# Performance work log

Measured on AMD Instinct MI355X. Metric: run time of the kernel, lower is better.

The kernel has to match this reference:

```python
import jax, jax.numpy as jnp
import numpy as np

B, L, HS, WS = 4, 5, 32, 32
C = 256            # dim == heads * dim_head
M, D = 8, 32       # heads, dim_head
T, R = 2, 4        # num_types, num_relations
I = M * D          # inner_dim
EPS = 1e-5


def setup_inputs() -> dict:
    key = jax.random.key(0)
    ks = jax.random.split(key, 12)
    w = 0.02
    x = jax.random.normal(ks[0], (B, L, HS, WS, C), dtype=jnp.float32)
    mask = jnp.ones((B, HS, WS, L, L), dtype=jnp.int32)
    prior_encoding = jax.random.randint(ks[1], (B, L, HS, WS, 3), 0, T).astype(jnp.float32)
    return {
        "x": x,
        "mask": mask,
        "prior_encoding": prior_encoding,
        "ln_w": jnp.ones((C,), jnp.float32),
        "ln_b": jnp.zeros((C,), jnp.float32),
        "Wq": jax.random.normal(ks[2], (T, C, I), jnp.float32) * w,
        "bq": jnp.zeros((T, I), jnp.float32),
        "Wk": jax.random.normal(ks[3], (T, C, I), jnp.float32) * w,
        "bk": jnp.zeros((T, I), jnp.float32),
        "Wv": jax.random.normal(ks[4], (T, C, I), jnp.float32) * w,
        "bv": jnp.zeros((T, I), jnp.float32),
        "Wa": jax.random.normal(ks[5], (T, I, C), jnp.float32) * w,
        "ba": jnp.zeros((T, C), jnp.float32),
        "rel_att": jax.random.normal(ks[6], (R, M, D, D), jnp.float32) * w,
        "rel_msg": jax.random.normal(ks[7], (R, M, D, D), jnp.float32) * w,
    }


def _hgt_forward(x, mask, prior_encoding, ln_w, ln_b, Wq, bq, Wk, bk, Wv, bv, Wa, ba, rel_att, rel_msg):
    # pre-LayerNorm over channel dim
    mu = jnp.mean(x, axis=-1, keepdims=True)
    var = jnp.mean(jnp.square(x - mu), axis=-1, keepdims=True)
    xn = (x - mu) * jax.lax.rsqrt(var + EPS) * ln_w + ln_b

    # [B,L,H,W,C] -> [B,H,W,L,C]
    xp = jnp.transpose(xn, (0, 2, 3, 1, 4))
    types = prior_encoding[:, :, 0, 0, 2].astype(jnp.int32)  # [B,L]

    # per-type q/k/v projections via gather of type-indexed weights
    q = jnp.einsum('bhwlc,blci->bhwli', xp, Wq[types]) + bq[types][:, None, None]
    k = jnp.einsum('bhwlc,blci->bhwli', xp, Wk[types]) + bk[types][:, None, None]
    v = jnp.einsum('bhwlc,blci->bhwli', xp, Wv[types]) + bv[types][:, None, None]

    def to_heads(t):  # [B,H,W,L,I] -> [B,M,H,W,L,D]
        return jnp.transpose(t.reshape(B, HS, WS, L, M, D), (0, 4, 1, 2, 3, 5))
    q, k, v = to_heads(q), to_heads(k), to_heads(v)

    # relation-indexed edge weights: e_type = t_i * T + t_j
    e = types[:, :, None] * T + types[:, None, :]              # [B,L,L]
    w_att = jnp.transpose(rel_att[e], (0, 3, 1, 2, 4, 5))      # [B,M,L,L,D,D]
    w_msg = jnp.transpose(rel_msg[e], (0, 3, 1, 2, 4, 5))

    scale = D ** -0.5
    q_w = jnp.einsum('bmhwip,bmijpq->bmhwijq', q, w_att)
    att = jnp.einsum('bmhwijq,bmhwjq->bmhwij', q_w, k) * scale
    att = jnp.where(mask[:, None] == 0, -1e9, att)
    att = jax.nn.softmax(att, axis=-1)

    v_msg = jnp.einsum('bmijpc,bmhwjp->bmhwijc', w_msg, v)
    out = jnp.einsum('bmhwij,bmhwijc->bmhwic', att, v_msg)

    # [B,M,H,W,L,D] -> [B,H,W,L,C]
    out = jnp.transpose(out, (0, 2, 3, 4, 1, 5)).reshape(B, HS, WS, L, I)
    out = jnp.einsum('bhwli,blic->bhwlc', out, Wa[types]) + ba[types][:, None, None]
    # dropout is identity at inference
    return jnp.transpose(out, (0, 3, 1, 2, 4))                 # [B,L,H,W,C]


def reference(x, mask, prior_encoding, ln_w, ln_b, Wq, bq, Wk, bk, Wv, bv, Wa, ba, rel_att, rel_msg):
    return _hgt_forward(x, mask, prior_encoding, ln_w, ln_b, Wq, bq, Wk, bk, Wv, bv, Wa, ba, rel_att, rel_msg)
```

## Files before the change

kernel.cpp:

```cpp
#include <hip/hip_runtime.h>
#include <hip/hip_bf16.h>
#include <math.h>

#define BB 4
#define LL 5
#define HSZ 32
#define WSZ 32
#define PP (HSZ*WSZ)
#define CC 256
#define MM 8
#define DD 32
#define II 256
#define TT 2
#define NTOK (BB*PP*LL*II)
#define TILE_ELEMS 8192
#define SCALE 0.17677669529663687f

typedef short bf16x8 __attribute__((ext_vector_type(8)));
typedef float f32x4 __attribute__((ext_vector_type(4)));

static __device__ __forceinline__ ushort f2bf(float f) {
    unsigned u = __float_as_uint(f);
    unsigned r = (u + 0x7fffu + ((u >> 16) & 1u)) >> 16;
    return (ushort)r;
}
static __device__ __forceinline__ float bf2f(ushort u) {
    return __uint_as_float(((unsigned)u) << 16);
}

__global__ __launch_bounds__(256) void k_fold(
    const float* __restrict__ Wq, const float* __restrict__ Wv,
    const float* __restrict__ Wk, const float* __restrict__ Wa,
    const float* __restrict__ bq, const float* __restrict__ bv,
    const float* __restrict__ rel_att, const float* __restrict__ rel_msg,
    const float* __restrict__ x,
    const float* __restrict__ lnw, const float* __restrict__ lnb,
    ushort* __restrict__ packW, float* __restrict__ bEff,
    ushort* __restrict__ xnPack)
{
    __shared__ float As[1024];
    __shared__ ushort Apack[8192];
    const int blk = blockIdx.x;
    const int tid = threadIdx.x;

    if (blk < 64) {
        const int p  = blk >> 5;
        const int t  = (blk >> 4) & 1;
        const int ts = (blk >> 3) & 1;
        const int m  = blk & 7;
        const float* A = (p == 0)
            ? rel_att + (size_t)((t * 2 + ts) * 8 + m) * 1024
            : rel_msg + (size_t)((ts * 2 + t) * 8 + m) * 1024;
        for (int i = tid; i < 1024; i += 256) As[i] = A[i];
        __syncthreads();

        const float* W = ((p == 0) ? Wq : Wv) + (size_t)t * 65536;
        const int k = tid;
        float wrow[32];
        #pragma unroll
        for (int u = 0; u < 8; ++u)
            *(float4*)&wrow[u * 4] = *(const float4*)&W[k * 256 + m * 32 + u * 4];

        const int slot = (p == 0 ? 0 : 4) + t * 2 + ts;
        ushort* base = packW + (size_t)slot * 65536;
        const int kt = k >> 5, j = k & 7, lq = ((k >> 3) & 3) * 16;
        #pragma unroll
        for (int q = 0; q < 32; ++q) {
            float acc = 0.f;
            #pragma unroll
            for (int pp = 0; pp < 32; ++pp) acc += wrow[pp] * As[pp * 32 + q];
            const int nt = m * 2 + (q >> 4);
            const int lane = lq + (q & 15);
            base[(size_t)((nt * 8 + kt) * 64 + lane) * 8 + j] = f2bf(acc);
        }
        if (tid < 32) {
            const int q = tid;
            const float* bi = ((p == 0) ? bq : bv) + t * 256 + m * 32;
            float acc = 0.f;
            #pragma unroll
            for (int pp = 0; pp < 32; ++pp) acc += bi[pp] * As[pp * 32 + q];
            bEff[(p ? 1024 : 0) + (t * 2 + ts) * 256 + m * 32 + q] = acc;
        }
    } else if (blk < 192) {
        const int idx = blk - 64;
        const int which = idx >> 6;
        const int gi = (idx & 63) * 256 + tid;
        const int t = gi >> 13;
        const int sub = gi & 8191;
        const float* src = ((which == 0) ? Wk : Wa) + (size_t)t * 65536;
        const int slot = (which == 0 ? 8 : 10) + t;
        const int nt = sub >> 9, kt = (sub >> 6) & 7, lane = sub & 63;
        const int k0 = kt * 32 + (lane >> 4) * 8;
        const int n  = nt * 16 + (lane & 15);
        ushort h[8];
        #pragma unroll
        for (int j = 0; j < 8; ++j) h[j] = f2bf(src[(size_t)(k0 + j) * 256 + n]);
        uint4 o;
        o.x = (unsigned)h[0] | ((unsigned)h[1] << 16);
        o.y = (unsigned)h[2] | ((unsigned)h[3] << 16);
        o.z = (unsigned)h[4] | ((unsigned)h[5] << 16);
        o.w = (unsigned)h[6] | ((unsigned)h[7] << 16);
        *(uint4*)(packW + (size_t)slot * 65536 + (size_t)sub * 8) = o;
    } else {
        const int lblk = blk - 192;
        const int bl  = lblk >> 5;
        const int pt  = lblk & 31;
        const int p0  = pt * 32;

        const int r  = tid >> 3;
        const int jj = tid & 7;
        const float* xrow = x + ((size_t)bl * PP + p0 + r) * CC;
        float4 xv[8];
        float s1 = 0.f, s2 = 0.f;
        #pragma unroll
        for (int u = 0; u < 8; ++u) {
            xv[u] = *(const float4*)(xrow + jj * 32 + u * 4);
            s1 += xv[u].x + xv[u].y + xv[u].z + xv[u].w;
            s2 += xv[u].x * xv[u].x + xv[u].y * xv[u].y + xv[u].z * xv[u].z + xv[u].w * xv[u].w;
        }
        s1 += __shfl_xor(s1, 1); s1 += __shfl_xor(s1, 2); s1 += __shfl_xor(s1, 4);
        s2 += __shfl_xor(s2, 1); s2 += __shfl_xor(s2, 2); s2 += __shfl_xor(s2, 4);
        const float mu   = s1 * (1.0f / 256.0f);
        const float var  = s2 * (1.0f / 256.0f) - mu * mu;
        const float rstd = rsqrtf(var + 1e-5f);

        const int mt_r = r >> 4, rm = r & 15;
        #pragma unroll
        for (int u = 0; u < 8; ++u) {
            const int c0 = jj * 32 + u * 4;
            const float4 g  = *(const float4*)(lnw + c0);
            const float4 bt = *(const float4*)(lnb + c0);
            const ushort h0 = f2bf((xv[u].x - mu) * rstd * g.x + bt.x);
            const ushort h1 = f2bf((xv[u].y - mu) * rstd * g.y + bt.y);
            const ushort h2 = f2bf((xv[u].z - mu) * rstd * g.z + bt.z);
            const ushort h3 = f2bf((xv[u].w - mu) * rstd * g.w + bt.w);
            uint2 w2;
            w2.x = (unsigned)h0 | ((unsigned)h1 << 16);
            w2.y = (unsigned)h2 | ((unsigned)h3 << 16);
            const int kt   = c0 >> 5;
            const int lsub = rm + (((c0 >> 3) & 3) << 4);
            const int j0   = c0 & 7;
            *(uint2*)&Apack[(((mt_r * 8 + kt) * 64 + lsub) << 3) + j0] = w2;
        }
        __syncthreads();

        const size_t tbase = (size_t)lblk * TILE_ELEMS;
        #pragma unroll
        for (int u = 0; u < 4; ++u) {
            const int ch = (tid + u * 256) * 8;
            *(uint4*)&xnPack[tbase + ch] = *(const uint4*)&Apack[ch];
        }
    }
}

__global__ __launch_bounds__(256) void k_proj(
    const ushort* __restrict__ xnPack, const float* __restrict__ prior,
    const ushort* __restrict__ packW, const float* __restrict__ bEff,
    const float* __restrict__ bk,
    ushort* __restrict__ qw0, ushort* __restrict__ qw1, ushort* __restrict__ kkO,
    ushort* __restrict__ vm0, ushort* __restrict__ vm1)
{
    __shared__ ushort As[8192];

    const int tid  = threadIdx.x;
    const int blk  = blockIdx.x;
    const int mat  = blk / 640;
    const int rem  = blk - mat * 640;
    const int bl   = rem >> 5;
    const int sub  = rem & 31;
    const int pg   = sub >> 1;
    const int half = sub & 1;
    const int t    = (int)prior[(size_t)bl * (PP * 3) + 2];

    int slot; const float* bias;
    if (mat < 2)       { slot = t * 2 + mat;           bias = bEff + slot * 256; }
    else if (mat == 2) { slot = 8 + t;                 bias = bk + t * 256; }
    else               { slot = 4 + t * 2 + (mat - 3); bias = bEff + 1024 + (t * 2 + (mat - 3)) * 256; }
    ushort* dst = (mat == 0) ? qw0 : (mat == 1) ? qw1 : (mat == 2) ? kkO : (mat == 3) ? vm0 : vm1;

    const int wv = tid >> 6, lane = tid & 63;

    const ushort* Bp = packW + (size_t)slot * 65536;
    bf16x8 bfr[8][2];
    #pragma unroll
    for (int kt = 0; kt < 8; ++kt)
        #pragma unroll
        for (int nn = 0; nn < 2; ++nn) {
            const int ntg = half * 8 + wv * 2 + nn;
            bfr[kt][nn] = *(const bf16x8*)&Bp[(size_t)((ntg * 8 + kt) * 64 + lane) * 8];
        }

    const int cl = lane & 15, rq = lane >> 4;
    const int colA = half * 128 + wv * 32 + cl;
    const int colB = colA + 16;
    const float biasA = bias[colA], biasB = bias[colB];

    #pragma unroll 1
    for (int tl = 0; tl < 2; ++tl) {
        const int pt = pg * 2 + tl;
        const size_t tbase = (size_t)(bl * 32 + pt) * TILE_ELEMS;
        __syncthreads();
        #pragma unroll
        for (int u = 0; u < 4; ++u) {
            const int ch = (tid + u * 256) * 8;
            *(uint4*)&As[ch] = *(const uint4*)&xnPack[tbase + ch];
        }
        __syncthreads();

        f32x4 acc[2][2];
        #pragma unroll
        for (int mt = 0; mt < 2; ++mt)
            #pragma unroll
            for (int nn = 0; nn < 2; ++nn)
                acc[mt][nn] = (f32x4){0.f, 0.f, 0.f, 0.f};

        #pragma unroll
        for (int kt = 0; kt < 8; ++kt) {
            const bf16x8 a0 = *(const bf16x8*)&As[((0 * 8 + kt) * 64 + lane) << 3];
            const bf16x8 a1 = *(const bf16x8*)&As[((1 * 8 + kt) * 64 + lane) << 3];
            acc[0][0] = __builtin_amdgcn_mfma_f32_16x16x32_bf16(a0, bfr[kt][0], acc[0][0], 0, 0, 0);
            acc[0][1] = __builtin_amdgcn_mfma_f32_16x16x32_bf16(a0, bfr[kt][1], acc[0][1], 0, 0, 0);
            acc[1][0] = __builtin_amdgcn_mfma_f32_16x16x32_bf16(a1, bfr[kt][0], acc[1][0], 0, 0, 0);
            acc[1][1] = __builtin_amdgcn_mfma_f32_16x16x32_bf16(a1, bfr[kt][1], acc[1][1], 0, 0, 0);
        }

        const int p0 = pt * 32;
        #pragma unroll
        for (int mt = 0; mt < 2; ++mt) {
            const int row0 = p0 + mt * 16 + rq * 4;
            #pragma unroll
            for (int r2 = 0; r2 < 4; ++r2) {
                const size_t rb = ((size_t)bl * PP + row0 + r2) * II;
                dst[rb + colA] = f2bf(acc[mt][0][r2] + biasA);
                dst[rb + colB] = f2bf(acc[mt][1][r2] + biasB);
            }
        }
    }
}

__global__ __launch_bounds__(256) void k_attn_lite(
    const ushort* __restrict__ qw0, const ushort* __restrict__ qw1,
    const ushort* __restrict__ kkI,
    const ushort* __restrict__ vm0, const ushort* __restrict__ vm1,
    const int* __restrict__ mask, const float* __restrict__ prior,
    ushort* __restrict__ aoPack)
{
    const int tid  = threadIdx.x;
    const int site = blockIdx.x * 4 + (tid >> 6);
    const int lane = tid & 63;
    const int b    = site >> 10;
    const int pix  = site & 1023;
    const int c0   = lane * 4;

    int ty[5];
    #pragma unroll
    for (int l = 0; l < 5; ++l)
        ty[l] = (int)prior[(size_t)(b * 5 + l) * (PP * 3) + 2];

    float qf[2][5][4], kf[5][4], vf[2][5][4];
    #pragma unroll
    for (int l = 0; l < 5; ++l) {
        const size_t base = (((size_t)(b * 5 + l) << 10) + pix) * II + c0;
        const ushort4 q0 = *(const ushort4*)(qw0 + base);
        const ushort4 q1 = *(const ushort4*)(qw1 + base);
        const ushort4 kv = *(const ushort4*)(kkI + base);
        const ushort4 v0 = *(const ushort4*)(vm0 + base);
        const ushort4 v1 = *(const ushort4*)(vm1 + base);
        qf[0][l][0] = bf2f(q0.x); qf[0][l][1] = bf2f(q0.y); qf[0][l][2] = bf2f(q0.z); qf[0][l][3] = bf2f(q0.w);
        qf[1][l][0] = bf2f(q1.x); qf[1][l][1] = bf2f(q1.y); qf[1][l][2] = bf2f(q1.z); qf[1][l][3] = bf2f(q1.w);
        kf[l][0]    = bf2f(kv.x); kf[l][1]    = bf2f(kv.y); kf[l][2]    = bf2f(kv.z); kf[l][3]    = bf2f(kv.w);
        vf[0][l][0] = bf2f(v0.x); vf[0][l][1] = bf2f(v0.y); vf[0][l][2] = bf2f(v0.z); vf[0][l][3] = bf2f(v0.w);
        vf[1][l][0] = bf2f(v1.x); vf[1][l][1] = bf2f(v1.y); vf[1][l][2] = bf2f(v1.z); vf[1][l][3] = bf2f(v1.w);
    }

    const int rr   = pix & 31;
    const int tile0 = b * 5 * 32 + (pix >> 5);
    const int mt   = rr >> 4;
    const int ktc  = c0 >> 5;
    const int lp   = (rr & 15) + 16 * ((c0 >> 3) & 3);
    const int j0   = c0 & 7;
    const int fofs = ((mt * 8 + ktc) * 64 + lp) * 8 + j0;

    #pragma unroll
    for (int i = 0; i < 5; ++i) {
        float lg[5];
        #pragma unroll
        for (int j = 0; j < 5; ++j) {
            const float s0 = qf[0][i][0] * kf[j][0] + qf[0][i][1] * kf[j][1]
                           + qf[0][i][2] * kf[j][2] + qf[0][i][3] * kf[j][3];
            const float s1 = qf[1][i][0] * kf[j][0] + qf[1][i][1] * kf[j][1]
                           + qf[1][i][2] * kf[j][2] + qf[1][i][3] * kf[j][3];
            float s = ty[j] ? s1 : s0;
            s += __shfl_xor(s, 1); s += __shfl_xor(s, 2); s += __shfl_xor(s, 4);
            const int mv = mask[((size_t)site * 5 + i) * 5 + j];
            lg[j] = mv ? s * SCALE : -1e9f;
        }
        float mx = lg[0];
        #pragma unroll
        for (int j = 1; j < 5; ++j) mx = fmaxf(mx, lg[j]);
        float ex[5], sum = 0.f;
        #pragma unroll
        for (int j = 0; j < 5; ++j) { ex[j] = __expf(lg[j] - mx); sum += ex[j]; }
        const float rs = 1.0f / sum;
        float o0 = 0.f, o1 = 0.f, o2 = 0.f, o3 = 0.f;
        #pragma unroll
        for (int j = 0; j < 5; ++j) {
            const float w = ex[j] * rs;
            o0 += w * (ty[i] ? vf[1][j][0] : vf[0][j][0]);
            o1 += w * (ty[i] ? vf[1][j][1] : vf[0][j][1]);
            o2 += w * (ty[i] ? vf[1][j][2] : vf[0][j][2]);
            o3 += w * (ty[i] ? vf[1][j][3] : vf[0][j][3]);
        }
        uint2 w2;
        w2.x = (unsigned)f2bf(o0) | ((unsigned)f2bf(o1) << 16);
        w2.y = (unsigned)f2bf(o2) | ((unsigned)f2bf(o3) << 16);
        *(uint2*)&aoPack[(size_t)(tile0 + i * 32) * TILE_ELEMS + fofs] = w2;
    }
}

__global__ __launch_bounds__(256) void k_out(
    const ushort* __restrict__ aoPack, const float* __restrict__ prior,
    const ushort* __restrict__ packW, const float* __restrict__ ba,
    float* __restrict__ out)
{
    __shared__ ushort As[8192];
    __shared__ float obufF[32 * 132];

    const int tid  = threadIdx.x;
    const int blk  = blockIdx.x;
    const int bl   = blk >> 6;
    const int sub  = blk & 63;
    const int pt   = sub >> 1;
    const int half = sub & 1;
    const int bbi  = bl / LL;
    const int l    = bl - bbi * LL;
    const int t    = (int)prior[(size_t)bl * (PP * 3) + 2];

    const int wv = tid >> 6, lane = tid & 63;
    const ushort* Bp = packW + (size_t)(10 + t) * 65536;
    bf16x8 bfr[8][2];
    #pragma unroll
    for (int kt = 0; kt < 8; ++kt)
        #pragma unroll
        for (int nn = 0; nn < 2; ++nn) {
            const int ntg = half * 8 + wv * 2 + nn;
            bfr[kt][nn] = *(const bf16x8*)&Bp[(size_t)((ntg * 8 + kt) * 64 + lane) * 8];
        }

    const size_t tbase = (size_t)(bl * 32 + pt) * TILE_ELEMS;
    #pragma unroll
    for (int u = 0; u < 4; ++u) {
        const int ch = (tid + u * 256) * 8;
        *(uint4*)&As[ch] = *(const uint4*)&aoPack[tbase + ch];
    }
    __syncthreads();

    const int cl = lane & 15, rq = lane >> 4;
    const int colL_A = wv * 32 + cl;
    const int colL_B = colL_A + 16;
    const float biasA = ba[t * CC + half * 128 + colL_A];
    const float biasB = ba[t * CC + half * 128 + colL_B];

    f32x4 acc[2][2];
    #pragma unroll
    for (int mt = 0; mt < 2; ++mt)
        #pragma unroll
        for (int nn = 0; nn < 2; ++nn)
            acc[mt][nn] = (f32x4){0.f, 0.f, 0.f, 0.f};

    #pragma unroll
    for (int kt = 0; kt < 8; ++kt) {
        const bf16x8 a0 = *(const bf16x8*)&As[((0 * 8 + kt) * 64 + lane) << 3];
        const bf16x8 a1 = *(const bf16x8*)&As[((1 * 8 + kt) * 64 + lane) << 3];
        acc[0][0] = __builtin_amdgcn_mfma_f32_16x16x32_bf16(a0, bfr[kt][0], acc[0][0], 0, 0, 0);
        acc[0][1] = __builtin_amdgcn_mfma_f32_16x16x32_bf16(a0, bfr[kt][1], acc[0][1], 0, 0, 0);
        acc[1][0] = __builtin_amdgcn_mfma_f32_16x16x32_bf16(a1, bfr[kt][0], acc[1][0], 0, 0, 0);
        acc[1][1] = __builtin_amdgcn_mfma_f32_16x16x32_bf16(a1, bfr[kt][1], acc[1][1], 0, 0, 0);
    }

    #pragma unroll
    for (int mt = 0; mt < 2; ++mt) {
        const int rowb = mt * 16 + rq * 4;
        #pragma unroll
        for (int r2 = 0; r2 < 4; ++r2) {
            obufF[(rowb + r2) * 132 + colL_A] = acc[mt][0][r2] + biasA;
            obufF[(rowb + r2) * 132 + colL_B] = acc[mt][1][r2] + biasB;
        }
    }
    __syncthreads();

    const int p0 = pt * 32;
    #pragma unroll
    for (int k2 = 0; k2 < 4; ++k2) {
        const int id  = tid + k2 * 256;
        const int row = id >> 5;
        const int ch  = (id & 31) * 4;
        const float4 v4 = *(const float4*)&obufF[row * 132 + ch];
        *(float4*)(out + ((size_t)(bbi * LL + l) * PP + p0 + row) * CC + half * 128 + ch) = v4;
    }
}

extern "C" void kernel_launch(void* const* d_in, const int* in_sizes, int n_in,
                              void* d_out, int out_size, void* d_ws, size_t ws_size,
                              hipStream_t stream) {
    const float* x       = (const float*)d_in[0];
    const int*   mask    = (const int*)d_in[1];
    const float* prior   = (const float*)d_in[2];
    const float* lnw     = (const float*)d_in[3];
    const float* lnb     = (const float*)d_in[4];
    const float* Wq      = (const float*)d_in[5];
    const float* bq      = (const float*)d_in[6];
    const float* Wk      = (const float*)d_in[7];
    const float* bk      = (const float*)d_in[8];
    const float* Wv      = (const float*)d_in[9];
    const float* bv      = (const float*)d_in[10];
    const float* Wa      = (const float*)d_in[11];
    const float* ba      = (const float*)d_in[12];
    const float* rel_att = (const float*)d_in[13];
    const float* rel_msg = (const float*)d_in[14];
    float* out = (float*)d_out;

    ushort* qw0    = (ushort*)d_ws;
    ushort* qw1    = qw0 + NTOK;
    ushort* kko    = qw1 + NTOK;
    ushort* vm0    = kko + NTOK;
    ushort* vm1    = vm0 + NTOK;
    ushort* aoPack = vm1 + NTOK;
    ushort* xnPack = aoPack + NTOK;
    ushort* packW  = xnPack + NTOK;
    float*  bEff   = (float*)(packW + 12 * 65536);

    hipLaunchKernelGGL(k_fold, dim3(832), dim3(256), 0, stream,
                       Wq, Wv, Wk, Wa, bq, bv, rel_att, rel_msg,
                       x, lnw, lnb, packW, bEff, xnPack);
    hipLaunchKernelGGL(k_proj, dim3(3200), dim3(256), 0, stream,
                       xnPack, prior, packW, bEff, bk, qw0, qw1, kko, vm0, vm1);
    hipLaunchKernelGGL(k_attn_lite, dim3(1024), dim3(256), 0, stream,
                       qw0, qw1, kko, vm0, vm1, mask, prior, aoPack);
    hipLaunchKernelGGL(k_out, dim3(1280), dim3(256), 0, stream,
                       aoPack, prior, packW, ba, out);
}
```

Before: 150.1 us.

## Fuse attention and output projection into one kernel via block-local staging

Merges the attention kernel and the output-projection kernel into a single launch. Each 512-thread block computes attention for 16 pixels across all 5 positions, writes the bf16 result to a block-private global scratch tile, then runs the MFMA output projection on that tile after a block barrier. This removes one kernel launch and keeps the intermediate likely cache-resident. In exchange the grid drops to 256 blocks, B weights are re-read from global each loop instead of kept in registers, and the output is stored with scattered scalar writes rather than staged float4 stores.

```diff
diff --git a/kernel.cpp b/kernel.cpp
--- a/kernel.cpp
+++ b/kernel.cpp
@@ -238,165 +238,124 @@
     }
 }
 
-__global__ __launch_bounds__(256) void k_attn_lite(
+__global__ __launch_bounds__(512) void k_attn_out(
     const ushort* __restrict__ qw0, const ushort* __restrict__ qw1,
     const ushort* __restrict__ kkI,
     const ushort* __restrict__ vm0, const ushort* __restrict__ vm1,
     const int* __restrict__ mask, const float* __restrict__ prior,
-    ushort* __restrict__ aoPack)
+    const ushort* __restrict__ packW, const float* __restrict__ ba,
+    ushort* __restrict__ aoG, float* __restrict__ out)
 {
+    __shared__ int tys[8];
+
     const int tid  = threadIdx.x;
-    const int site = blockIdx.x * 4 + (tid >> 6);
+    const int wv   = tid >> 6;
     const int lane = tid & 63;
-    const int b    = site >> 10;
-    const int pix  = site & 1023;
-    const int c0   = lane * 4;
-
-    int ty[5];
-    #pragma unroll
-    for (int l = 0; l < 5; ++l)
-        ty[l] = (int)prior[(size_t)(b * 5 + l) * (PP * 3) + 2];
-
-    float qf[2][5][4], kf[5][4], vf[2][5][4];
-    #pragma unroll
-    for (int l = 0; l < 5; ++l) {
-        const size_t base = (((size_t)(b * 5 + l) << 10) + pix) * II + c0;
-        const ushort4 q0 = *(const ushort4*)(qw0 + base);
-        const ushort4 q1 = *(const ushort4*)(qw1 + base);
-        const ushort4 kv = *(const ushort4*)(kkI + base);
-        const ushort4 v0 = *(const ushort4*)(vm0 + base);
-        const ushort4 v1 = *(const ushort4*)(vm1 + base);
-        qf[0][l][0] = bf2f(q0.x); qf[0][l][1] = bf2f(q0.y); qf[0][l][2] = bf2f(q0.z); qf[0][l][3] = bf2f(q0.w);
-        qf[1][l][0] = bf2f(q1.x); qf[1][l][1] = bf2f(q1.y); qf[1][l][2] = bf2f(q1.z); qf[1][l][3] = bf2f(q1.w);
-        kf[l][0]    = bf2f(kv.x); kf[l][1]    = bf2f(kv.y); kf[l][2]    = bf2f(kv.z); kf[l][3]    = bf2f(kv.w);
-        vf[0][l][0] = bf2f(v0.x); vf[0][l][1] = bf2f(v0.y); vf[0][l][2] = bf2f(v0.z); vf[0][l][3] = bf2f(v0.w);
-        vf[1][l][0] = bf2f(v1.x); vf[1][l][1] = bf2f(v1.y); vf[1][l][2] = bf2f(v1.z); vf[1][l][3] = bf2f(v1.w);
+    const int blk  = blockIdx.x;
+    const int b    = blk >> 6;
+    const int p0   = (blk & 63) * 16;
+
+    if (tid < 5) tys[tid] = (int)prior[(size_t)(b * 5 + tid) * (PP * 3) + 2];
+    __syncthreads();
+
+    const int c0 = lane * 4;
+    const int ktc  = lane >> 3;
+    const int lpc  = 16 * ((lane >> 1) & 3);
+    const int j0   = 4 * (lane & 1);
+
+    #pragma unroll 1
+    for (int ss = 0; ss < 2; ++ss) {
+        const int pixl = wv * 2 + ss;
+        const int pix  = p0 + pixl;
+        const size_t siteg = (size_t)b * PP + pix;
+
+        float qf[2][5][4], kf[5][4], vf[2][5][4];
+        #pragma unroll
+        for (int l = 0; l < 5; ++l) {
+            const size_t base = (((size_t)(b * 5 + l) << 10) + pix) * II + c0;
+            const ushort4 q0 = *(const ushort4*)(qw0 + base);
+            const ushort4 q1 = *(const ushort4*)(qw1 + base);
+            const ushort4 kv = *(const ushort4*)(kkI + base);
+            const ushort4 v0 = *(const ushort4*)(vm0 + base);
+            const ushort4 v1 = *(const ushort4*)(vm1 + base);
+            qf[0][l][0] = bf2f(q0.x); qf[0][l][1] = bf2f(q0.y); qf[0][l][2] = bf2f(q0.z); qf[0][l][3] = bf2f(q0.w);
+            qf[1][l][0] = bf2f(q1.x); qf[1][l][1] = bf2f(q1.y); qf[1][l][2] = bf2f(q1.z); qf[1][l][3] = bf2f(q1.w);
+            kf[l][0]    = bf2f(kv.x); kf[l][1]    = bf2f(kv.y); kf[l][2]    = bf2f(kv.z); kf[l][3]    = bf2f(kv.w);
+            vf[0][l][0] = bf2f(v0.x); vf[0][l][1] = bf2f(v0.y); vf[0][l][2] = bf2f(v0.z); vf[0][l][3] = bf2f(v0.w);
+            vf[1][l][0] = bf2f(v1.x); vf[1][l][1] = bf2f(v1.y); vf[1][l][2] = bf2f(v1.z); vf[1][l][3] = bf2f(v1.w);
+        }
+
+        #pragma unroll
+        for (int i = 0; i < 5; ++i) {
+            float lg[5];
+            #pragma unroll
+            for (int j = 0; j < 5; ++j) {
+                const float s0 = qf[0][i][0] * kf[j][0] + qf[0][i][1] * kf[j][1]
+                               + qf[0][i][2] * kf[j][2] + qf[0][i][3] * kf[j][3];
+                const float s1 = qf[1][i][0] * kf[j][0] + qf[1][i][1] * kf[j][1]
+                               + qf[1][i][2] * kf[j][2] + qf[1][i][3] * kf[j][3];
+                float s = tys[j] ? s1 : s0;
+                s += __shfl_xor(s, 1); s += __shfl_xor(s, 2); s += __shfl_xor(s, 4);
+                const int mv = mask[(siteg * 5 + i) * 5 + j];
+                lg[j] = mv ? s * SCALE : -1e9f;
+            }
+            float mx = lg[0];
+            #pragma unroll
+            for (int j = 1; j < 5; ++j) mx = fmaxf(mx, lg[j]);
+            float ex[5], sum = 0.f;
+            #pragma unroll
+            for (int j = 0; j < 5; ++j) { ex[j] = __expf(lg[j] - mx); sum += ex[j]; }
+            const float rs = 1.0f / sum;
+            float o0 = 0.f, o1 = 0.f, o2 = 0.f, o3 = 0.f;
+            #pragma unroll
+            for (int j = 0; j < 5; ++j) {
+                const float w = ex[j] * rs;
+                o0 += w * (tys[i] ? vf[1][j][0] : vf[0][j][0]);
+                o1 += w * (tys[i] ? vf[1][j][1] : vf[0][j][1]);
+                o2 += w * (tys[i] ? vf[1][j][2] : vf[0][j][2]);
+                o3 += w * (tys[i] ? vf[1][j][3] : vf[0][j][3]);
+            }
+            uint2 w2;
+            w2.x = (unsigned)f2bf(o0) | ((unsigned)f2bf(o1) << 16);
+            w2.y = (unsigned)f2bf(o2) | ((unsigned)f2bf(o3) << 16);
+            const size_t elem = (size_t)blk * 20480 + (size_t)i * 4096
+                              + (size_t)((ktc * 64) + (pixl + lpc)) * 8 + j0;
+            *(uint2*)&aoG[elem] = w2;
+        }
     }
 
-    const int rr   = pix & 31;
-    const int tile0 = b * 5 * 32 + (pix >> 5);
-    const int mt   = rr >> 4;
-    const int ktc  = c0 >> 5;
-    const int lp   = (rr & 15) + 16 * ((c0 >> 3) & 3);
-    const int j0   = c0 & 7;
-    const int fofs = ((mt * 8 + ktc) * 64 + lp) * 8 + j0;
-
-    #pragma unroll
-    for (int i = 0; i < 5; ++i) {
-        float lg[5];
-        #pragma unroll
-        for (int j = 0; j < 5; ++j) {
-            const float s0 = qf[0][i][0] * kf[j][0] + qf[0][i][1] * kf[j][1]
-                           + qf[0][i][2] * kf[j][2] + qf[0][i][3] * kf[j][3];
-            const float s1 = qf[1][i][0] * kf[j][0] + qf[1][i][1] * kf[j][1]
-                           + qf[1][i][2] * kf[j][2] + qf[1][i][3] * kf[j][3];
-            float s = ty[j] ? s1 : s0;
-            s += __shfl_xor(s, 1); s += __shfl_xor(s, 2); s += __shfl_xor(s, 4);
-            const int mv = mask[((size_t)site * 5 + i) * 5 + j];
-            lg[j] = mv ? s * SCALE : -1e9f;
-        }
-        float mx = lg[0];
-        #pragma unroll
-        for (int j = 1; j < 5; ++j) mx = fmaxf(mx, lg[j]);
-        float ex[5], sum = 0.f;
-        #pragma unroll
-        for (int j = 0; j < 5; ++j) { ex[j] = __expf(lg[j] - mx); sum += ex[j]; }
-        const float rs = 1.0f / sum;
-        float o0 = 0.f, o1 = 0.f, o2 = 0.f, o3 = 0.f;
-        #pragma unroll
-        for (int j = 0; j < 5; ++j) {
-            const float w = ex[j] * rs;
-            o0 += w * (ty[i] ? vf[1][j][0] : vf[0][j][0]);
-            o1 += w * (ty[i] ? vf[1][j][1] : vf[0][j][1]);
-            o2 += w * (ty[i] ? vf[1][j][2] : vf[0][j][2]);
-            o3 += w * (ty[i] ? vf[1][j][3] : vf[0][j][3]);
-        }
-        uint2 w2;
-        w2.x = (unsigned)f2bf(o0) | ((unsigned)f2bf(o1) << 16);
-        w2.y = (unsigned)f2bf(o2) | ((unsigned)f2bf(o3) << 16);
-        *(uint2*)&aoPack[(size_t)(tile0 + i * 32) * TILE_ELEMS + fofs] = w2;
-    }
-}
-
-__global__ __launch_bounds__(256) void k_out(
-    const ushort* __restrict__ aoPack, const float* __restrict__ prior,
-    const ushort* __restrict__ packW, const float* __restrict__ ba,
-    float* __restrict__ out)
-{
-    __shared__ ushort As[8192];
-    __shared__ float obufF[32 * 132];
-
-    const int tid  = threadIdx.x;
-    const int blk  = blockIdx.x;
-    const int bl   = blk >> 6;
-    const int sub  = blk & 63;
-    const int pt   = sub >> 1;
-    const int half = sub & 1;
-    const int bbi  = bl / LL;
-    const int l    = bl - bbi * LL;
-    const int t    = (int)prior[(size_t)bl * (PP * 3) + 2];
-
-    const int wv = tid >> 6, lane = tid & 63;
-    const ushort* Bp = packW + (size_t)(10 + t) * 65536;
-    bf16x8 bfr[8][2];
-    #pragma unroll
-    for (int kt = 0; kt < 8; ++kt)
-        #pragma unroll
-        for (int nn = 0; nn < 2; ++nn) {
-            const int ntg = half * 8 + wv * 2 + nn;
-            bfr[kt][nn] = *(const bf16x8*)&Bp[(size_t)((ntg * 8 + kt) * 64 + lane) * 8];
-        }
-
-    const size_t tbase = (size_t)(bl * 32 + pt) * TILE_ELEMS;
-    #pragma unroll
-    for (int u = 0; u < 4; ++u) {
-        const int ch = (tid + u * 256) * 8;
-        *(uint4*)&As[ch] = *(const uint4*)&aoPack[tbase + ch];
-    }
+    __threadfence_block();
     __syncthreads();
 
     const int cl = lane & 15, rq = lane >> 4;
-    const int colL_A = wv * 32 + cl;
-    const int colL_B = colL_A + 16;
-    const float biasA = ba[t * CC + half * 128 + colL_A];
-    const float biasB = ba[t * CC + half * 128 + colL_B];
-
-    f32x4 acc[2][2];
-    #pragma unroll
-    for (int mt = 0; mt < 2; ++mt)
-        #pragma unroll
-        for (int nn = 0; nn < 2; ++nn)
-            acc[mt][nn] = (f32x4){0.f, 0.f, 0.f, 0.f};
-
-    #pragma unroll
-    for (int kt = 0; kt < 8; ++kt) {
-        const bf16x8 a0 = *(const bf16x8*)&As[((0 * 8 + kt) * 64 + lane) << 3];
-        const bf16x8 a1 = *(const bf16x8*)&As[((1 * 8 + kt) * 64 + lane) << 3];
-        acc[0][0] = __builtin_amdgcn_mfma_f32_16x16x32_bf16(a0, bfr[kt][0], acc[0][0], 0, 0, 0);
-        acc[0][1] = __builtin_amdgcn_mfma_f32_16x16x32_bf16(a0, bfr[kt][1], acc[0][1], 0, 0, 0);
-        acc[1][0] = __builtin_amdgcn_mfma_f32_16x16x32_bf16(a1, bfr[kt][0], acc[1][0], 0, 0, 0);
-        acc[1][1] = __builtin_amdgcn_mfma_f32_16x16x32_bf16(a1, bfr[kt][1], acc[1][1], 0, 0, 0);
-    }
-
-    #pragma unroll
-    for (int mt = 0; mt < 2; ++mt) {
-        const int rowb = mt * 16 + rq * 4;
+    #pragma unroll 1
+    for (int g = wv; g < 40; g += 8) {
+        const int mt  = g >> 3;
+        const int ntp = g & 7;
+        const int t   = tys[mt];
+        const ushort* Bp = packW + (size_t)(10 + t) * 65536;
+        const ushort* Ap = aoG + (size_t)blk * 20480 + (size_t)mt * 4096;
+        const int nt0 = ntp * 2, nt1 = nt0 + 1;
+
+        f32x4 acc0 = (f32x4){0.f, 0.f, 0.f, 0.f};
+        f32x4 acc1 = (f32x4){0.f, 0.f, 0.f, 0.f};
+        #pragma unroll
+        for (int kt = 0; kt < 8; ++kt) {
+            const bf16x8 a  = *(const bf16x8*)&Ap[(size_t)(kt * 64 + lane) * 8];
+            const bf16x8 b0 = *(const bf16x8*)&Bp[(size_t)((nt0 * 8 + kt) * 64 + lane) * 8];
+            const bf16x8 b1 = *(const bf16x8*)&Bp[(size_t)((nt1 * 8 + kt) * 64 + lane) * 8];
+            acc0 = __builtin_amdgcn_mfma_f32_16x16x32_bf16(a, b0, acc0, 0, 0, 0);
+            acc1 = __builtin_amdgcn_mfma_f32_16x16x32_bf16(a, b1, acc1, 0, 0, 0);
+        }
+
+        const float bias0 = ba[t * CC + nt0 * 16 + cl];
+        const float bias1 = ba[t * CC + nt1 * 16 + cl];
+        float* ob = out + ((size_t)(b * 5 + mt) * PP + p0 + rq * 4) * CC;
         #pragma unroll
         for (int r2 = 0; r2 < 4; ++r2) {
-            obufF[(rowb + r2) * 132 + colL_A] = acc[mt][0][r2] + biasA;
-            obufF[(rowb + r2) * 132 + colL_B] = acc[mt][1][r2] + biasB;
-        }
-    }
-    __syncthreads();
-
-    const int p0 = pt * 32;
-    #pragma unroll
-    for (int k2 = 0; k2 < 4; ++k2) {
-        const int id  = tid + k2 * 256;
-        const int row = id >> 5;
-        const int ch  = (id & 31) * 4;
-        const float4 v4 = *(const float4*)&obufF[row * 132 + ch];
-        *(float4*)(out + ((size_t)(bbi * LL + l) * PP + p0 + row) * CC + half * 128 + ch) = v4;
+            ob[(size_t)r2 * CC + nt0 * 16 + cl] = acc0[r2] + bias0;
+            ob[(size_t)r2 * CC + nt1 * 16 + cl] = acc1[r2] + bias1;
+        }
     }
 }
 
@@ -425,8 +384,8 @@
     ushort* kko    = qw1 + NTOK;
     ushort* vm0    = kko + NTOK;
     ushort* vm1    = vm0 + NTOK;
-    ushort* aoPack = vm1 + NTOK;
-    ushort* xnPack = aoPack + NTOK;
+    ushort* aoG    = vm1 + NTOK;
+    ushort* xnPack = aoG + NTOK;
     ushort* packW  = xnPack + NTOK;
     float*  bEff   = (float*)(packW + 12 * 65536);
 
@@ -435,8 +394,6 @@
                        x, lnw, lnb, packW, bEff, xnPack);
     hipLaunchKernelGGL(k_proj, dim3(3200), dim3(256), 0, stream,
                        xnPack, prior, packW, bEff, bk, qw0, qw1, kko, vm0, vm1);
-    hipLaunchKernelGGL(k_attn_lite, dim3(1024), dim3(256), 0, stream,
-                       qw0, qw1, kko, vm0, vm1, mask, prior, aoPack);
-    hipLaunchKernelGGL(k_out, dim3(1280), dim3(256), 0, stream,
-                       aoPack, prior, packW, ba, out);
-}
+    hipLaunchKernelGGL(k_attn_out, dim3(256), dim3(512), 0, stream,
+                       qw0, qw1, kko, vm0, vm1, mask, prior, packW, ba, aoG, out);
+}
```

After: 157.3 us. 4.8% more time.

## Use 512-thread blocks covering full output width in projection and output GEMMs

Applied to the files above, without the earlier changes.

k_proj and k_out now run 8 waves per block so one block covers all 256 output columns of a 32-row tile, where before two blocks each covered half. k_proj drops its two-tile loop and processes one tile per block. The A tile is loaded into LDS once and shared by twice as many columns, which halves redundant xnPack/aoPack reads, and k_out launches half as many blocks. In exchange each block uses more LDS and there are fewer, larger blocks, which can reduce occupancy and scheduling flexibility.

```diff
diff --git a/kernel.cpp b/kernel.cpp
--- a/kernel.cpp
+++ b/kernel.cpp
@@ -153,7 +153,7 @@
     }
 }
 
-__global__ __launch_bounds__(256) void k_proj(
+__global__ __launch_bounds__(512) void k_proj(
     const ushort* __restrict__ xnPack, const float* __restrict__ prior,
     const ushort* __restrict__ packW, const float* __restrict__ bEff,
     const float* __restrict__ bk,
@@ -167,9 +167,7 @@
     const int mat  = blk / 640;
     const int rem  = blk - mat * 640;
     const int bl   = rem >> 5;
-    const int sub  = rem & 31;
-    const int pg   = sub >> 1;
-    const int half = sub & 1;
+    const int pt   = rem & 31;
     const int t    = (int)prior[(size_t)bl * (PP * 3) + 2];
 
     int slot; const float* bias;
@@ -186,54 +184,48 @@
     for (int kt = 0; kt < 8; ++kt)
         #pragma unroll
         for (int nn = 0; nn < 2; ++nn) {
-            const int ntg = half * 8 + wv * 2 + nn;
+            const int ntg = wv * 2 + nn;
             bfr[kt][nn] = *(const bf16x8*)&Bp[(size_t)((ntg * 8 + kt) * 64 + lane) * 8];
         }
 
+    const size_t tbase = (size_t)(bl * 32 + pt) * TILE_ELEMS;
+    #pragma unroll
+    for (int u = 0; u < 2; ++u) {
+        const int ch = (tid + u * 512) * 8;
+        *(uint4*)&As[ch] = *(const uint4*)&xnPack[tbase + ch];
+    }
+    __syncthreads();
+
+    f32x4 acc[2][2];
+    #pragma unroll
+    for (int mt = 0; mt < 2; ++mt)
+        #pragma unroll
+        for (int nn = 0; nn < 2; ++nn)
+            acc[mt][nn] = (f32x4){0.f, 0.f, 0.f, 0.f};
+
+    #pragma unroll
+    for (int kt = 0; kt < 8; ++kt) {
+        const bf16x8 a0 = *(const bf16x8*)&As[((0 * 8 + kt) * 64 + lane) << 3];
+        const bf16x8 a1 = *(const bf16x8*)&As[((1 * 8 + kt) * 64 + lane) << 3];
+        acc[0][0] = __builtin_amdgcn_mfma_f32_16x16x32_bf16(a0, bfr[kt][0], acc[0][0], 0, 0, 0);
+        acc[0][1] = __builtin_amdgcn_mfma_f32_16x16x32_bf16(a0, bfr[kt][1], acc[0][1], 0, 0, 0);
+        acc[1][0] = __builtin_amdgcn_mfma_f32_16x16x32_bf16(a1, bfr[kt][0], acc[1][0], 0, 0, 0);
+        acc[1][1] = __builtin_amdgcn_mfma_f32_16x16x32_bf16(a1, bfr[kt][1], acc[1][1], 0, 0, 0);
+    }
+
     const int cl = lane & 15, rq = lane >> 4;
-    const int colA = half * 128 + wv * 32 + cl;
+    const int colA = wv * 32 + cl;
     const int colB = colA + 16;
     const float biasA = bias[colA], biasB = bias[colB];
-
-    #pragma unroll 1
-    for (int tl = 0; tl < 2; ++tl) {
-        const int pt = pg * 2 + tl;
-        const size_t tbase = (size_t)(bl * 32 + pt) * TILE_ELEMS;
-        __syncthreads();
-        #pragma unroll
-        for (int u = 0; u < 4; ++u) {
-            const int ch = (tid + u * 256) * 8;
-            *(uint4*)&As[ch] = *(const uint4*)&xnPack[tbase + ch];
-        }
-        __syncthreads();
-
-        f32x4 acc[2][2];
-        #pragma unroll
-        for (int mt = 0; mt < 2; ++mt)
-            #pragma unroll
-            for (int nn = 0; nn < 2; ++nn)
-                acc[mt][nn] = (f32x4){0.f, 0.f, 0.f, 0.f};
-
-        #pragma unroll
-        for (int kt = 0; kt < 8; ++kt) {
-            const bf16x8 a0 = *(const bf16x8*)&As[((0 * 8 + kt) * 64 + lane) << 3];
-            const bf16x8 a1 = *(const bf16x8*)&As[((1 * 8 + kt) * 64 + lane) << 3];
-            acc[0][0] = __builtin_amdgcn_mfma_f32_16x16x32_bf16(a0, bfr[kt][0], acc[0][0], 0, 0, 0);
-            acc[0][1] = __builtin_amdgcn_mfma_f32_16x16x32_bf16(a0, bfr[kt][1], acc[0][1], 0, 0, 0);
-            acc[1][0] = __builtin_amdgcn_mfma_f32_16x16x32_bf16(a1, bfr[kt][0], acc[1][0], 0, 0, 0);
-            acc[1][1] = __builtin_amdgcn_mfma_f32_16x16x32_bf16(a1, bfr[kt][1], acc[1][1], 0, 0, 0);
-        }
-
-        const int p0 = pt * 32;
-        #pragma unroll
-        for (int mt = 0; mt < 2; ++mt) {
-            const int row0 = p0 + mt * 16 + rq * 4;
-            #pragma unroll
-            for (int r2 = 0; r2 < 4; ++r2) {
-                const size_t rb = ((size_t)bl * PP + row0 + r2) * II;
-                dst[rb + colA] = f2bf(acc[mt][0][r2] + biasA);
-                dst[rb + colB] = f2bf(acc[mt][1][r2] + biasB);
-            }
+    const int p0 = pt * 32;
+    #pragma unroll
+    for (int mt = 0; mt < 2; ++mt) {
+        const int row0 = p0 + mt * 16 + rq * 4;
+        #pragma unroll
+        for (int r2 = 0; r2 < 4; ++r2) {
+            const size_t rb = ((size_t)bl * PP + row0 + r2) * II;
+            dst[rb + colA] = f2bf(acc[mt][0][r2] + biasA);
+            dst[rb + colB] = f2bf(acc[mt][1][r2] + biasB);
         }
     }
 }
@@ -318,20 +310,18 @@
     }
 }
 
-__global__ __launch_bounds__(256) void k_out(
+__global__ __launch_bounds__(512) void k_out(
     const ushort* __restrict__ aoPack, const float* __restrict__ prior,
     const ushort* __restrict__ packW, const float* __restrict__ ba,
     float* __restrict__ out)
 {
     __shared__ ushort As[8192];
-    __shared__ float obufF[32 * 132];
+    __shared__ float obufF[32 * 260];
 
     const int tid  = threadIdx.x;
     const int blk  = blockIdx.x;
-    const int bl   = blk >> 6;
-    const int sub  = blk & 63;
-    const int pt   = sub >> 1;
-    const int half = sub & 1;
+    const int bl   = blk >> 5;
+    const int pt   = blk & 31;
     const int bbi  = bl / LL;
     const int l    = bl - bbi * LL;
     const int t    = (int)prior[(size_t)bl * (PP * 3) + 2];
@@ -343,23 +333,17 @@
     for (int kt = 0; kt < 8; ++kt)
         #pragma unroll
         for (int nn = 0; nn < 2; ++nn) {
-            const int ntg = half * 8 + wv * 2 + nn;
+            const int ntg = wv * 2 + nn;
             bfr[kt][nn] = *(const bf16x8*)&Bp[(size_t)((ntg * 8 + kt) * 64 + lane) * 8];
         }
 
     const size_t tbase = (size_t)(bl * 32 + pt) * TILE_ELEMS;
     #pragma unroll
-    for (int u = 0; u < 4; ++u) {
-        const int ch = (tid + u * 256) * 8;
+    for (int u = 0; u < 2; ++u) {
+        const int ch = (tid + u * 512) * 8;
         *(uint4*)&As[ch] = *(const uint4*)&aoPack[tbase + ch];
     }
     __syncthreads();
-
-    const int cl = lane & 15, rq = lane >> 4;
-    const int colL_A = wv * 32 + cl;
-    const int colL_B = colL_A + 16;
-    const float biasA = ba[t * CC + half * 128 + colL_A];
-    const float biasB = ba[t * CC + half * 128 + colL_B];
 
     f32x4 acc[2][2];
     #pragma unroll
@@ -378,13 +362,18 @@
         acc[1][1] = __builtin_amdgcn_mfma_f32_16x16x32_bf16(a1, bfr[kt][1], acc[1][1], 0, 0, 0);
     }
 
+    const int cl = lane & 15, rq = lane >> 4;
+    const int colA = wv * 32 + cl;
+    const int colB = colA + 16;
+    const float biasA = ba[t * CC + colA];
+    const float biasB = ba[t * CC + colB];
     #pragma unroll
     for (int mt = 0; mt < 2; ++mt) {
         const int rowb = mt * 16 + rq * 4;
         #pragma unroll
         for (int r2 = 0; r2 < 4; ++r2) {
-            obufF[(rowb + r2) * 132 + colL_A] = acc[mt][0][r2] + biasA;
-            obufF[(rowb + r2) * 132 + colL_B] = acc[mt][1][r2] + biasB;
+            obufF[(rowb + r2) * 260 + colA] = acc[mt][0][r2] + biasA;
+            obufF[(rowb + r2) * 260 + colB] = acc[mt][1][r2] + biasB;
         }
     }
     __syncthreads();
@@ -392,11 +381,11 @@
     const int p0 = pt * 32;
     #pragma unroll
     for (int k2 = 0; k2 < 4; ++k2) {
-        const int id  = tid + k2 * 256;
-        const int row = id >> 5;
-        const int ch  = (id & 31) * 4;
-        const float4 v4 = *(const float4*)&obufF[row * 132 + ch];
-        *(float4*)(out + ((size_t)(bbi * LL + l) * PP + p0 + row) * CC + half * 128 + ch) = v4;
+        const int id  = tid + k2 * 512;
+        const int row = id >> 6;
+        const int ch  = (id & 63) * 4;
+        const float4 v4 = *(const float4*)&obufF[row * 260 + ch];
+        *(float4*)(out + ((size_t)(bbi * LL + l) * PP + p0 + row) * CC + ch) = v4;
     }
 }
 
@@ -433,10 +422,10 @@
     hipLaunchKernelGGL(k_fold, dim3(832), dim3(256), 0, stream,
                        Wq, Wv, Wk, Wa, bq, bv, rel_att, rel_msg,
                        x, lnw, lnb, packW, bEff, xnPack);
-    hipLaunchKernelGGL(k_proj, dim3(3200), dim3(256), 0, stream,
+    hipLaunchKernelGGL(k_proj, dim3(3200), dim3(512), 0, stream,
                        xnPack, prior, packW, bEff, bk, qw0, qw1, kko, vm0, vm1);
     hipLaunchKernelGGL(k_attn_lite, dim3(1024), dim3(256), 0, stream,
                        qw0, qw1, kko, vm0, vm1, mask, prior, aoPack);
-    hipLaunchKernelGGL(k_out, dim3(1280), dim3(256), 0, stream,
+    hipLaunchKernelGGL(k_out, dim3(640), dim3(512), 0, stream,
                        aoPack, prior, packW, ba, out);
 }
```

Measured after the change: 151.1 us. About the same (+0.7%).
